# Optimization experiments

Hardware: AMD Instinct MI355X
Metric: run time of the kernel (lower is better)

## Reference

```python
import jax, jax.numpy as jnp
import numpy as np

DIM = 2048
H = 16          # query heads
KVH = 4         # kv heads
HD = 128        # head dim
GROUPS = H // KVH
ROPE_BASE = 10000.0


def _rope_cache(seq_len, head_dim):
    inv_freq = 1.0 / (ROPE_BASE ** (jnp.arange(0, head_dim, 2, dtype=jnp.float32) / head_dim))
    t = jnp.arange(seq_len, dtype=jnp.float32)
    freqs = jnp.outer(t, inv_freq)            # [N, hd/2]
    emb = jnp.concatenate([freqs, freqs], -1)  # [N, hd]
    return jnp.cos(emb), jnp.sin(emb)


def _apply_rope(x, cos, sin):
    # x: [B, H, N, hd]; cos/sin: [N, hd]
    hd = x.shape[-1]
    x1, x2 = x[..., : hd // 2], x[..., hd // 2:]
    rotated = jnp.concatenate([-x2, x1], -1)
    return x * cos[None, None] + rotated * sin[None, None]


def setup_inputs() -> dict:
    key = jax.random.key(0)
    ks = jax.random.split(key, 5)
    B, N = 2, 2048
    s = 0.02
    return {
        "x": jax.random.normal(ks[0], (B, N, DIM), jnp.float32),
        "Wq": jax.random.normal(ks[1], (DIM, H * HD), jnp.float32) * s,
        "Wk": jax.random.normal(ks[2], (DIM, KVH * HD), jnp.float32) * s,
        "Wv": jax.random.normal(ks[3], (DIM, KVH * HD), jnp.float32) * s,
        "Wo": jax.random.normal(ks[4], (H * HD, DIM), jnp.float32) * s,
    }


def reference(x, Wq, Wk, Wv, Wo):
    B, N, D = x.shape
    scale = HD ** -0.5
    q = (x @ Wq).reshape(B, N, H, HD).transpose(0, 2, 1, 3)      # [B,H,N,hd]
    k = (x @ Wk).reshape(B, N, KVH, HD).transpose(0, 2, 1, 3)    # [B,KVH,N,hd]
    v = (x @ Wv).reshape(B, N, KVH, HD).transpose(0, 2, 1, 3)
    # GQA expansion (done before RoPE, matching the original)
    k = jnp.repeat(k, GROUPS, axis=1)                            # [B,H,N,hd]
    v = jnp.repeat(v, GROUPS, axis=1)
    cos, sin = _rope_cache(N, HD)
    q = _apply_rope(q, cos, sin)
    k = _apply_rope(k, cos, sin)
    attn = jnp.einsum("bhqd,bhkd->bhqk", q, k) * scale           # [B,H,N,N]
    causal = jnp.tril(jnp.ones((N, N), dtype=bool))
    attn = jnp.where(causal[None, None], attn, -jnp.inf)
    attn = jax.nn.softmax(attn, axis=-1)
    out = jnp.einsum("bhqk,bhkd->bhqd", attn, v)                 # [B,H,N,hd]
    out = out.transpose(0, 2, 1, 3).reshape(B, N, H * HD)
    return out @ Wo
```

## Files before the change

kernel.cpp:

```cpp
#include <hip/hip_runtime.h>
#include <hip/hip_bf16.h>

#define DIM 2048
#define NH 16
#define KVH 4
#define HD 128
#define BATCH 2
#define SEQ 2048
#define MTOT (BATCH*SEQ)
#define SCALE 0.08838834764831845f
#define SCALE_L2E 0.12751743762f

using f32x4 = __attribute__((ext_vector_type(4))) float;
using s16x4 = __attribute__((ext_vector_type(4))) short;
using s16x8 = __attribute__((ext_vector_type(8))) short;
using bf16x8 = __attribute__((ext_vector_type(8))) __bf16;

__device__ inline short f2bf(float x) { __bf16 h = (__bf16)x; return __builtin_bit_cast(short, h); }
__device__ inline float bf2f(short s) { return (float)__builtin_bit_cast(__bf16, s); }

__device__ inline bf16x8 ld_frag128(const short* p) {
  return __builtin_bit_cast(bf16x8, *(const s16x8*)p);
}

__device__ inline bf16x8 ld_frag(const short* p) {
  s16x4 lo = *(const s16x4*)p;
  s16x4 hi = *(const s16x4*)(p + 16);
  s16x8 f = __builtin_shufflevector(lo, hi, 0, 1, 2, 3, 4, 5, 6, 7);
  return __builtin_bit_cast(bf16x8, f);
}

__device__ inline bf16x8 pack_p(f32x4 a, f32x4 b) {
  bf16x8 o;
  o[0] = (__bf16)a[0]; o[1] = (__bf16)a[1]; o[2] = (__bf16)a[2]; o[3] = (__bf16)a[3];
  o[4] = (__bf16)b[0]; o[5] = (__bf16)b[1]; o[6] = (__bf16)b[2]; o[7] = (__bf16)b[3];
  return o;
}


__global__ void k_rope_table(float* __restrict__ tab) {
  int n = blockIdx.x, i = threadIdx.x;
  float inv = expf(-(2.f * i / (float)HD) * logf(10000.f));
  float a = (float)n * inv;
  tab[n * HD + i] = cosf(a);
  tab[n * HD + 64 + i] = sinf(a);
}

__global__ void k_cvt_bf16(const float* __restrict__ in, short* __restrict__ out, int n4) {
  int i = blockIdx.x * 256 + threadIdx.x;
  if (i >= n4) return;
  f32x4 v = *(const f32x4*)(in + (size_t)i * 4);
  s16x4 o;
  o[0] = f2bf(v[0]); o[1] = f2bf(v[1]); o[2] = f2bf(v[2]); o[3] = f2bf(v[3]);
  *(s16x4*)(out + (size_t)i * 4) = o;
}

__global__ __launch_bounds__(256) void k_transpose(const float* __restrict__ W, short* __restrict__ WT,
                                                   int K, int N) {
  __shared__ float t[32][33];
  int n0 = blockIdx.x * 32, k0 = blockIdx.y * 32;
  int tx = threadIdx.x & 31, ty = threadIdx.x >> 5;
#pragma unroll
  for (int i = 0; i < 4; i++) t[ty + i * 8][tx] = W[(size_t)(k0 + ty + i * 8) * N + n0 + tx];
  __syncthreads();
#pragma unroll
  for (int i = 0; i < 4; i++) WT[(size_t)(n0 + ty + i * 8) * K + k0 + tx] = f2bf(t[tx][ty + i * 8]);
}

__global__ __launch_bounds__(256) void k_transpose_v(const short* __restrict__ v_r, short* __restrict__ v_t) {
  __shared__ short t[64][70];
  const int z = blockIdx.z;
  const int s0 = blockIdx.x * 64, d0 = blockIdx.y * 64;
  const long ibase = ((long)z * SEQ + s0) * HD + d0;
  const long obase = ((long)z * HD + d0) * SEQ + s0;
  const int tid = threadIdx.x;
#pragma unroll
  for (int c = 0; c < 4; c++) {
    int chunk = tid + c * 256;
    int row = chunk >> 4, col4 = (chunk & 15) * 4;
    *(s16x4*)&t[row][col4] = *(const s16x4*)(v_r + ibase + (long)row * HD + col4);
  }
  __syncthreads();
#pragma unroll
  for (int c = 0; c < 4; c++) {
    int chunk = tid + c * 256;
    int row = chunk >> 4, col4 = (chunk & 15) * 4;
    s16x4 o;
    o[0] = t[col4 + 0][row]; o[1] = t[col4 + 1][row];
    o[2] = t[col4 + 2][row]; o[3] = t[col4 + 3][row];
    *(s16x4*)(v_t + obase + (long)row * SEQ + col4) = o;
  }
}

template <int MODE, int HH>
__device__ inline void gemm_bt_body(const short* __restrict__ A, const short* __restrict__ BT,
                                    void* __restrict__ C, int M, int N, int K) {
  __shared__ short As[128 * 32];
  __shared__ short Bs[128 * 32];
  const int tid = threadIdx.x;
  const int wid = tid >> 6, lane = tid & 63;
  const int m0 = blockIdx.y * 128, n0 = blockIdx.x * 128;
  const int wr = wid >> 1, wc = wid & 1;
  const int l15 = lane & 15, g4 = (lane >> 4) * 4, kg8 = (lane >> 4) * 8;
  const int lrow = lane >> 2;
  const int lcol = (lane & 3) * 8;
  f32x4 acc[4][4] = {};

  for (int kt = 0; kt < K; kt += 32) {
    __syncthreads();
#pragma unroll
    for (int i = 0; i < 2; i++) {
      int r0 = wid * 32 + i * 16;
      const short* gp = A + (long)(m0 + r0 + lrow) * K + kt + lcol;
      __builtin_amdgcn_global_load_lds((const __attribute__((address_space(1))) void*)gp,
                                       (__attribute__((address_space(3))) void*)&As[r0 * 32], 16, 0, 0);
      const short* gq = BT + (long)(n0 + r0 + lrow) * K + kt + lcol;
      __builtin_amdgcn_global_load_lds((const __attribute__((address_space(1))) void*)gq,
                                       (__attribute__((address_space(3))) void*)&Bs[r0 * 32], 16, 0, 0);
    }
    __syncthreads();
    bf16x8 av[4];
#pragma unroll
    for (int mt = 0; mt < 4; mt++) av[mt] = ld_frag128(&As[(wr * 64 + mt * 16 + l15) * 32 + kg8]);
#pragma unroll
    for (int nt = 0; nt < 4; nt++) {
      bf16x8 bv = ld_frag128(&Bs[(wc * 64 + nt * 16 + l15) * 32 + kg8]);
#pragma unroll
      for (int mt = 0; mt < 4; mt++)
        acc[mt][nt] = __builtin_amdgcn_mfma_f32_16x16x32_bf16(av[mt], bv, acc[mt][nt], 0, 0, 0);
    }
  }

#pragma unroll
  for (int mt = 0; mt < 4; mt++) {
#pragma unroll
    for (int nt = 0; nt < 4; nt++) {
      int row = m0 + wr * 64 + mt * 16 + g4;
      int col = n0 + wc * 64 + nt * 16 + l15;
#pragma unroll
      for (int r = 0; r < 4; r++) {
        float v = acc[mt][nt][r];
        if (MODE == 0) {
          ((float*)C)[(long)(row + r) * N + col] = v;
        } else {
          int rg = row + r;
          int b = rg >> 11, n = rg & (SEQ - 1);
          int h = col >> 7, hd = col & (HD - 1);
          ((short*)C)[(((long)(b * HH + h)) * SEQ + n) * HD + hd] = f2bf(v);
        }
      }
    }
  }
}

__global__ __launch_bounds__(256) void k_gemm_q(const short* __restrict__ A, const short* __restrict__ BT,
                                                short* __restrict__ C, int M, int N, int K) {
  gemm_bt_body<1, NH>(A, BT, (void*)C, M, N, K);
}
__global__ __launch_bounds__(256) void k_gemm_kv(const short* __restrict__ A,
                                                 const short* __restrict__ BT0, const short* __restrict__ BT1,
                                                 short* __restrict__ C0, short* __restrict__ C1,
                                                 int M, int N, int K) {
  const short* BT = blockIdx.z ? BT1 : BT0;
  short* C = blockIdx.z ? C1 : C0;
  gemm_bt_body<1, KVH>(A, BT, (void*)C, M, N, K);
}
__global__ __launch_bounds__(256) void k_gemm_o(const short* __restrict__ A, const short* __restrict__ BT,
                                                float* __restrict__ C, int M, int N, int K) {
  gemm_bt_body<0, 0>(A, BT, (void*)C, M, N, K);
}

__global__ void k_rope(short* __restrict__ t, const float* __restrict__ tab, int total, float scale) {
  int idx = blockIdx.x * 256 + threadIdx.x;
  if (idx >= total) return;
  int i = idx & 63;
  int n = (idx >> 6) & (SEQ - 1);
  long base = (long)(idx >> 6) * HD;
  float c = tab[n * HD + i], s = tab[n * HD + 64 + i];
  float x1 = bf2f(t[base + i]), x2 = bf2f(t[base + 64 + i]);
  t[base + i] = f2bf((x1 * c - x2 * s) * scale);
  t[base + 64 + i] = f2bf((x2 * c + x1 * s) * scale);
}

__global__ __launch_bounds__(256, 2) void k_attn(const short* __restrict__ q_r, const short* __restrict__ k_r,
                                                 const short* __restrict__ v_t, short* __restrict__ attn_out) {
  __shared__ short Kl[64 * 136];
  __shared__ short Vt[128 * 68];
  const int tid = threadIdx.x, wid = tid >> 6, lane = tid & 63;
  const int l15 = lane & 15, g4 = (lane >> 4) * 4, kg8 = (lane >> 4) * 8;
  const int qlo = blockIdx.x;
  const int qhi = 31 - qlo;
  const int bh = blockIdx.y;
  const int b = bh >> 4, h = bh & 15, kvh = h >> 2;

  const long hbase = ((long)(b * NH + h)) * SEQ;
  bf16x8 aqL[4], aqH[4];
#pragma unroll
  for (int kt = 0; kt < 4; kt++) {
    aqL[kt] = ld_frag128(q_r + (hbase + qlo * 64 + wid * 16 + l15) * HD + kt * 32 + kg8);
    aqH[kt] = ld_frag128(q_r + (hbase + qhi * 64 + wid * 16 + l15) * HD + kt * 32 + kg8);
  }

  f32x4 accL[8] = {}, accH[8] = {};
  float mL = -1e30f, lL = 0.f, mH = -1e30f, lH = 0.f;
  const long kvbase = ((long)(b * KVH + kvh)) * SEQ * HD;
  const long vtbase = ((long)(b * KVH + kvh)) * HD * SEQ;
  const int qgL = qlo * 64 + wid * 16 + l15;
  const int qgH = qhi * 64 + wid * 16 + l15;

  s16x8 kreg[4], vreg[4];
#pragma unroll
  for (int c = 0; c < 4; c++) {
    int chunk = tid + c * 256;
    int kr = chunk >> 4, kc = (chunk & 15) * 8;
    kreg[c] = *(const s16x8*)(k_r + kvbase + (long)kr * HD + kc);
    int vr = chunk >> 3, vc = (chunk & 7) * 8;
    vreg[c] = *(const s16x8*)(v_t + vtbase + (long)vr * SEQ + vc);
  }

  for (int t64 = 0; t64 <= qhi; t64++) {
    __syncthreads();
#pragma unroll
    for (int c = 0; c < 4; c++) {
      int chunk = tid + c * 256;
      int kr = chunk >> 4, kc = (chunk & 15) * 8;
      *(s16x8*)&Kl[kr * 136 + kc] = kreg[c];
      int vr = chunk >> 3, vc = (chunk & 7) * 8;
      *(s16x8*)&Vt[vr * 68 + vc] = vreg[c];
    }
    __syncthreads();

    if (t64 < qhi) {
      const int kv0n = (t64 + 1) * 64;
#pragma unroll
      for (int c = 0; c < 4; c++) {
        int chunk = tid + c * 256;
        int kr = chunk >> 4, kc = (chunk & 15) * 8;
        kreg[c] = *(const s16x8*)(k_r + kvbase + (long)(kv0n + kr) * HD + kc);
        int vr = chunk >> 3, vc = (chunk & 7) * 8;
        vreg[c] = *(const s16x8*)(v_t + vtbase + (long)vr * SEQ + kv0n + vc);
      }
    }

    const int kv0 = t64 * 64;
    const bool actL = (t64 <= qlo);

    f32x4 sH[4] = {}, sL[4] = {};
#pragma unroll
    for (int nt = 0; nt < 4; nt++) {
#pragma unroll
      for (int kt = 0; kt < 4; kt++) {
        bf16x8 bk = ld_frag128(&Kl[(nt * 16 + l15) * 136 + kt * 32 + kg8]);
        sH[nt] = __builtin_amdgcn_mfma_f32_16x16x32_bf16(bk, aqH[kt], sH[nt], 0, 0, 0);
        if (actL) sL[nt] = __builtin_amdgcn_mfma_f32_16x16x32_bf16(bk, aqL[kt], sL[nt], 0, 0, 0);
      }
    }

    if (t64 == qhi) {
#pragma unroll
      for (int nt = 0; nt < 4; nt++) {
        int kvb = kv0 + nt * 16 + g4;
#pragma unroll
        for (int r = 0; r < 4; r++) sH[nt][r] = (kvb + r > qgH) ? -1e30f : sH[nt][r];
      }
    }
    if (actL && t64 == qlo) {
#pragma unroll
      for (int nt = 0; nt < 4; nt++) {
        int kvb = kv0 + nt * 16 + g4;
#pragma unroll
        for (int r = 0; r < 4; r++) sL[nt][r] = (kvb + r > qgL) ? -1e30f : sL[nt][r];
      }
    }

    {
      float tm = -1e30f;
#pragma unroll
      for (int nt = 0; nt < 4; nt++)
        tm = fmaxf(tm, fmaxf(fmaxf(sH[nt][0], sH[nt][1]), fmaxf(sH[nt][2], sH[nt][3])));
      tm = fmaxf(tm, __shfl_xor(tm, 16));
      tm = fmaxf(tm, __shfl_xor(tm, 32));
      if (!__all(tm - mH <= 8.f)) {
        float mn = fmaxf(mH, tm);
        float corr = exp2f(mH - mn);
        mH = mn;
        lH *= corr;
        float corr_r[4];
#pragma unroll
        for (int r = 0; r < 4; r++) corr_r[r] = __shfl(corr, g4 + r);
#pragma unroll
        for (int dt = 0; dt < 8; dt++)
#pragma unroll
          for (int r = 0; r < 4; r++) accH[dt][r] *= corr_r[r];
      }
      float rs = 0.f;
#pragma unroll
      for (int nt = 0; nt < 4; nt++)
#pragma unroll
        for (int r = 0; r < 4; r++) {
          float p = exp2f(sH[nt][r] - mH);
          sH[nt][r] = p;
          rs += p;
        }
      rs += __shfl_xor(rs, 16);
      rs += __shfl_xor(rs, 32);
      lH += rs;
      bf16x8 pa0 = pack_p(sH[0], sH[1]);
      bf16x8 pa1 = pack_p(sH[2], sH[3]);
#pragma unroll
      for (int dt = 0; dt < 8; dt++) {
        bf16x8 bv0 = ld_frag(&Vt[(dt * 16 + l15) * 68 + g4]);
        accH[dt] = __builtin_amdgcn_mfma_f32_16x16x32_bf16(pa0, bv0, accH[dt], 0, 0, 0);
        bf16x8 bv1 = ld_frag(&Vt[(dt * 16 + l15) * 68 + 32 + g4]);
        accH[dt] = __builtin_amdgcn_mfma_f32_16x16x32_bf16(pa1, bv1, accH[dt], 0, 0, 0);
      }
    }

    if (actL) {
      float tm = -1e30f;
#pragma unroll
      for (int nt = 0; nt < 4; nt++)
        tm = fmaxf(tm, fmaxf(fmaxf(sL[nt][0], sL[nt][1]), fmaxf(sL[nt][2], sL[nt][3])));
      tm = fmaxf(tm, __shfl_xor(tm, 16));
      tm = fmaxf(tm, __shfl_xor(tm, 32));
      if (!__all(tm - mL <= 8.f)) {
        float mn = fmaxf(mL, tm);
        float corr = exp2f(mL - mn);
        mL = mn;
        lL *= corr;
        float corr_r[4];
#pragma unroll
        for (int r = 0; r < 4; r++) corr_r[r] = __shfl(corr, g4 + r);
#pragma unroll
        for (int dt = 0; dt < 8; dt++)
#pragma unroll
          for (int r = 0; r < 4; r++) accL[dt][r] *= corr_r[r];
      }
      float rs = 0.f;
#pragma unroll
      for (int nt = 0; nt < 4; nt++)
#pragma unroll
        for (int r = 0; r < 4; r++) {
          float p = exp2f(sL[nt][r] - mL);
          sL[nt][r] = p;
          rs += p;
        }
      rs += __shfl_xor(rs, 16);
      rs += __shfl_xor(rs, 32);
      lL += rs;
      bf16x8 pa0 = pack_p(sL[0], sL[1]);
      bf16x8 pa1 = pack_p(sL[2], sL[3]);
#pragma unroll
      for (int dt = 0; dt < 8; dt++) {
        bf16x8 bv0 = ld_frag(&Vt[(dt * 16 + l15) * 68 + g4]);
        accL[dt] = __builtin_amdgcn_mfma_f32_16x16x32_bf16(pa0, bv0, accL[dt], 0, 0, 0);
        bf16x8 bv1 = ld_frag(&Vt[(dt * 16 + l15) * 68 + 32 + g4]);
        accL[dt] = __builtin_amdgcn_mfma_f32_16x16x32_bf16(pa1, bv1, accL[dt], 0, 0, 0);
      }
    }
  }

  {
    float inv = 1.f / lH;
    float inv_r[4];
#pragma unroll
    for (int r = 0; r < 4; r++) inv_r[r] = __shfl(inv, g4 + r);
    const long obase = ((long)(b * SEQ + qhi * 64 + wid * 16 + g4)) * (NH * HD) + (long)h * HD;
#pragma unroll
    for (int r = 0; r < 4; r++)
#pragma unroll
      for (int dt = 0; dt < 8; dt++)
        attn_out[obase + (long)r * (NH * HD) + dt * 16 + l15] = f2bf(accH[dt][r] * inv_r[r]);
  }
  {
    float inv = 1.f / lL;
    float inv_r[4];
#pragma unroll
    for (int r = 0; r < 4; r++) inv_r[r] = __shfl(inv, g4 + r);
    const long obase = ((long)(b * SEQ + qlo * 64 + wid * 16 + g4)) * (NH * HD) + (long)h * HD;
#pragma unroll
    for (int r = 0; r < 4; r++)
#pragma unroll
      for (int dt = 0; dt < 8; dt++)
        attn_out[obase + (long)r * (NH * HD) + dt * 16 + l15] = f2bf(accL[dt][r] * inv_r[r]);
  }
}

extern "C" void kernel_launch(void* const* d_in, const int* in_sizes, int n_in,
                              void* d_out, int out_size, void* d_ws, size_t ws_size,
                              hipStream_t stream) {
  const float* x = (const float*)d_in[0];
  const float* Wq = (const float*)d_in[1];
  const float* Wk = (const float*)d_in[2];
  const float* Wv = (const float*)d_in[3];
  const float* Wo = (const float*)d_in[4];

  char* w = (char*)d_ws;
  float* ropetab = (float*)w;  w += (size_t)SEQ * HD * 4;
  short* xb  = (short*)w;  w += (size_t)MTOT * DIM * 2;
  short* WqT = (short*)w;  w += (size_t)DIM * DIM * 2;
  short* WkT = (short*)w;  w += (size_t)(KVH * HD) * DIM * 2;
  short* WvT = (short*)w;  w += (size_t)(KVH * HD) * DIM * 2;
  short* WoT = (short*)w;  w += (size_t)DIM * DIM * 2;
  short* q_r = (short*)w;  w += (size_t)BATCH * NH * SEQ * HD * 2;
  short* k_r = (short*)w;  w += (size_t)BATCH * KVH * SEQ * HD * 2;
  short* v_r = (short*)w;  w += (size_t)BATCH * KVH * SEQ * HD * 2;
  short* attn = (short*)w; w += (size_t)MTOT * DIM * 2;
  short* v_t = xb;

  k_rope_table<<<SEQ, 64, 0, stream>>>(ropetab);
  k_cvt_bf16<<<(MTOT * DIM / 4 + 255) / 256, 256, 0, stream>>>(x, xb, MTOT * DIM / 4);
  k_transpose<<<dim3(DIM / 32, DIM / 32), 256, 0, stream>>>(Wq, WqT, DIM, DIM);
  k_transpose<<<dim3((KVH * HD) / 32, DIM / 32), 256, 0, stream>>>(Wk, WkT, DIM, KVH * HD);
  k_transpose<<<dim3((KVH * HD) / 32, DIM / 32), 256, 0, stream>>>(Wv, WvT, DIM, KVH * HD);
  k_transpose<<<dim3(DIM / 32, DIM / 32), 256, 0, stream>>>(Wo, WoT, DIM, DIM);

  k_gemm_q<<<dim3(DIM / 128, MTOT / 128), 256, 0, stream>>>(xb, WqT, q_r, MTOT, DIM, DIM);
  k_gemm_kv<<<dim3((KVH * HD) / 128, MTOT / 128, 2), 256, 0, stream>>>(xb, WkT, WvT, k_r, v_r,
                                                                       MTOT, KVH * HD, DIM);
  k_transpose_v<<<dim3(SEQ / 64, HD / 64, BATCH * KVH), 256, 0, stream>>>(v_r, v_t);
  k_rope<<<(BATCH * NH * SEQ * 64 + 255) / 256, 256, 0, stream>>>(q_r, ropetab, BATCH * NH * SEQ * 64, SCALE_L2E);
  k_rope<<<(BATCH * KVH * SEQ * 64 + 255) / 256, 256, 0, stream>>>(k_r, ropetab, BATCH * KVH * SEQ * 64, 1.0f);

  k_attn<<<dim3(SEQ / 128, BATCH * NH), 256, 0, stream>>>(q_r, k_r, v_t, attn);
  k_gemm_o<<<dim3(DIM / 128, MTOT / 128), 256, 0, stream>>>(attn, WoT, (float*)d_out, MTOT, DIM, DIM);
}
```

Measured before the change: 361.3 us.

## Double-buffer GEMM LDS tiles and fuse Q/K/V projections into one GEMM

The shared GEMM core now keeps two LDS buffers. It issues the global-to-LDS load for the next K-slice before computing on the current one, so load latency overlaps MFMA work and one barrier per slice is removed. The Q, K and V projections become a single launch over the concatenated transposed weights, which sit contiguously in the workspace. A lambda epilogue routes each column to the q, k or v head-major buffer. This doubles LDS use per block and relies on barriers draining the async LDS loads.

```diff
diff --git a/kernel.cpp b/kernel.cpp
--- a/kernel.cpp
+++ b/kernel.cpp
@@ -8,6 +8,7 @@
 #define BATCH 2
 #define SEQ 2048
 #define MTOT (BATCH*SEQ)
+#define NQKV (NH*HD + 2*KVH*HD)
 #define SCALE 0.08838834764831845f
 #define SCALE_L2E 0.12751743762f
 
@@ -92,11 +93,11 @@
   }
 }
 
-template <int MODE, int HH>
-__device__ inline void gemm_bt_body(const short* __restrict__ A, const short* __restrict__ BT,
-                                    void* __restrict__ C, int M, int N, int K) {
-  __shared__ short As[128 * 32];
-  __shared__ short Bs[128 * 32];
+template <class Epi>
+__device__ inline void gemm_core(const short* __restrict__ A, const short* __restrict__ BT,
+                                 int K, Epi epi) {
+  __shared__ short As[2][128 * 32];
+  __shared__ short Bs[2][128 * 32];
   const int tid = threadIdx.x;
   const int wid = tid >> 6, lane = tid & 63;
   const int m0 = blockIdx.y * 128, n0 = blockIdx.x * 128;
@@ -106,68 +107,76 @@
   const int lcol = (lane & 3) * 8;
   f32x4 acc[4][4] = {};
 
-  for (int kt = 0; kt < K; kt += 32) {
-    __syncthreads();
+  const long abase = (long)(m0 + lrow) * K + lcol;
+  const long bbase = (long)(n0 + lrow) * K + lcol;
+
+  auto stage = [&](int buf, int kt) {
 #pragma unroll
     for (int i = 0; i < 2; i++) {
       int r0 = wid * 32 + i * 16;
-      const short* gp = A + (long)(m0 + r0 + lrow) * K + kt + lcol;
+      const short* gp = A + abase + (long)r0 * K + kt;
       __builtin_amdgcn_global_load_lds((const __attribute__((address_space(1))) void*)gp,
-                                       (__attribute__((address_space(3))) void*)&As[r0 * 32], 16, 0, 0);
-      const short* gq = BT + (long)(n0 + r0 + lrow) * K + kt + lcol;
+                                       (__attribute__((address_space(3))) void*)&As[buf][r0 * 32], 16, 0, 0);
+      const short* gq = BT + bbase + (long)r0 * K + kt;
       __builtin_amdgcn_global_load_lds((const __attribute__((address_space(1))) void*)gq,
-                                       (__attribute__((address_space(3))) void*)&Bs[r0 * 32], 16, 0, 0);
-    }
-    __syncthreads();
+                                       (__attribute__((address_space(3))) void*)&Bs[buf][r0 * 32], 16, 0, 0);
+    }
+  };
+  auto compute = [&](int buf) {
     bf16x8 av[4];
 #pragma unroll
-    for (int mt = 0; mt < 4; mt++) av[mt] = ld_frag128(&As[(wr * 64 + mt * 16 + l15) * 32 + kg8]);
+    for (int mt = 0; mt < 4; mt++) av[mt] = ld_frag128(&As[buf][(wr * 64 + mt * 16 + l15) * 32 + kg8]);
 #pragma unroll
     for (int nt = 0; nt < 4; nt++) {
-      bf16x8 bv = ld_frag128(&Bs[(wc * 64 + nt * 16 + l15) * 32 + kg8]);
+      bf16x8 bv = ld_frag128(&Bs[buf][(wc * 64 + nt * 16 + l15) * 32 + kg8]);
 #pragma unroll
       for (int mt = 0; mt < 4; mt++)
         acc[mt][nt] = __builtin_amdgcn_mfma_f32_16x16x32_bf16(av[mt], bv, acc[mt][nt], 0, 0, 0);
     }
-  }
-
-#pragma unroll
-  for (int mt = 0; mt < 4; mt++) {
+  };
+
+  const int nk = K >> 5;
+  stage(0, 0);
+  __syncthreads();
+  for (int t = 0; t < nk; t += 2) {
+    if (t + 1 < nk) stage(1, (t + 1) << 5);
+    compute(0);
+    __syncthreads();
+    if (t + 2 < nk) stage(0, (t + 2) << 5);
+    compute(1);
+    __syncthreads();
+  }
+
+#pragma unroll
+  for (int mt = 0; mt < 4; mt++)
 #pragma unroll
     for (int nt = 0; nt < 4; nt++) {
       int row = m0 + wr * 64 + mt * 16 + g4;
       int col = n0 + wc * 64 + nt * 16 + l15;
 #pragma unroll
-      for (int r = 0; r < 4; r++) {
-        float v = acc[mt][nt][r];
-        if (MODE == 0) {
-          ((float*)C)[(long)(row + r) * N + col] = v;
-        } else {
-          int rg = row + r;
-          int b = rg >> 11, n = rg & (SEQ - 1);
-          int h = col >> 7, hd = col & (HD - 1);
-          ((short*)C)[(((long)(b * HH + h)) * SEQ + n) * HD + hd] = f2bf(v);
-        }
-      }
-    }
-  }
-}
-
-__global__ __launch_bounds__(256) void k_gemm_q(const short* __restrict__ A, const short* __restrict__ BT,
-                                                short* __restrict__ C, int M, int N, int K) {
-  gemm_bt_body<1, NH>(A, BT, (void*)C, M, N, K);
-}
-__global__ __launch_bounds__(256) void k_gemm_kv(const short* __restrict__ A,
-                                                 const short* __restrict__ BT0, const short* __restrict__ BT1,
-                                                 short* __restrict__ C0, short* __restrict__ C1,
-                                                 int M, int N, int K) {
-  const short* BT = blockIdx.z ? BT1 : BT0;
-  short* C = blockIdx.z ? C1 : C0;
-  gemm_bt_body<1, KVH>(A, BT, (void*)C, M, N, K);
-}
+      for (int r = 0; r < 4; r++) epi(row + r, col, acc[mt][nt][r]);
+    }
+}
+
+__global__ __launch_bounds__(256) void k_gemm_qkv(const short* __restrict__ A, const short* __restrict__ BT,
+                                                  short* __restrict__ q_r, short* __restrict__ k_r,
+                                                  short* __restrict__ v_r, int K) {
+  gemm_core(A, BT, K, [=](int row, int col, float v) {
+    int b = row >> 11, n = row & (SEQ - 1);
+    int hd = col & (HD - 1);
+    short* dst; long hb;
+    if (col < NH * HD) { dst = q_r; hb = b * NH + (col >> 7); }
+    else if (col < NH * HD + KVH * HD) { dst = k_r; hb = b * KVH + ((col - NH * HD) >> 7); }
+    else { dst = v_r; hb = b * KVH + ((col - NH * HD - KVH * HD) >> 7); }
+    dst[(hb * SEQ + n) * HD + hd] = f2bf(v);
+  });
+}
+
 __global__ __launch_bounds__(256) void k_gemm_o(const short* __restrict__ A, const short* __restrict__ BT,
-                                                float* __restrict__ C, int M, int N, int K) {
-  gemm_bt_body<0, 0>(A, BT, (void*)C, M, N, K);
+                                                float* __restrict__ C, int N, int K) {
+  gemm_core(A, BT, K, [=](int row, int col, float v) {
+    C[(long)row * N + col] = v;
+  });
 }
 
 __global__ void k_rope(short* __restrict__ t, const float* __restrict__ tab, int total, float scale) {
@@ -415,13 +424,11 @@
   k_transpose<<<dim3((KVH * HD) / 32, DIM / 32), 256, 0, stream>>>(Wv, WvT, DIM, KVH * HD);
   k_transpose<<<dim3(DIM / 32, DIM / 32), 256, 0, stream>>>(Wo, WoT, DIM, DIM);
 
-  k_gemm_q<<<dim3(DIM / 128, MTOT / 128), 256, 0, stream>>>(xb, WqT, q_r, MTOT, DIM, DIM);
-  k_gemm_kv<<<dim3((KVH * HD) / 128, MTOT / 128, 2), 256, 0, stream>>>(xb, WkT, WvT, k_r, v_r,
-                                                                       MTOT, KVH * HD, DIM);
+  k_gemm_qkv<<<dim3(NQKV / 128, MTOT / 128), 256, 0, stream>>>(xb, WqT, q_r, k_r, v_r, DIM);
   k_transpose_v<<<dim3(SEQ / 64, HD / 64, BATCH * KVH), 256, 0, stream>>>(v_r, v_t);
   k_rope<<<(BATCH * NH * SEQ * 64 + 255) / 256, 256, 0, stream>>>(q_r, ropetab, BATCH * NH * SEQ * 64, SCALE_L2E);
   k_rope<<<(BATCH * KVH * SEQ * 64 + 255) / 256, 256, 0, stream>>>(k_r, ropetab, BATCH * KVH * SEQ * 64, 1.0f);
 
   k_attn<<<dim3(SEQ / 128, BATCH * NH), 256, 0, stream>>>(q_r, k_r, v_t, attn);
-  k_gemm_o<<<dim3(DIM / 128, MTOT / 128), 256, 0, stream>>>(attn, WoT, (float*)d_out, MTOT, DIM, DIM);
-}
+  k_gemm_o<<<dim3(DIM / 128, MTOT / 128), 256, 0, stream>>>(attn, WoT, (float*)d_out, DIM, DIM);
+}
```

Measured after the change: 327.0 us. -9.5%, faster.
